# Optimization experiments

Measured on AMD Instinct MI355X. Metric: run time of the kernel, lower is better.

## Reference

```python
import jax, jax.numpy as jnp
import numpy as np

POS_R = 2
CELL_D = 16
BORDER = 16
B, D, H, W = 4, 128, 512, 512

# neighbourhood offsets with i*i + j*j <= pos_r^2, same ordering as the torch module
_OFFS = jnp.array([(i, j) for i in range(-POS_R, POS_R + 1)
                   for j in range(-POS_R, POS_R + 1)
                   if i * i + j * j <= POS_R ** 2], dtype=jnp.int32).T  # [2, K=13]


def _sample(det, max_b=None):
    # per-cell argmax of detection score; equivalent to pixel_unshuffle + argmax + coord gather
    Bt = det.shape[0] if max_b is None else min(max_b, det.shape[0])
    Hc = (H - 2 * BORDER) // CELL_D
    Wc = (W - 2 * BORDER) // CELL_D
    d = det[:Bt, 0, BORDER:BORDER + Hc * CELL_D, BORDER:BORDER + Wc * CELL_D]
    d = d.reshape(Bt, Hc, CELL_D, Wc, CELL_D).transpose(0, 1, 3, 2, 4)
    d = d.reshape(Bt, Hc, Wc, CELL_D * CELL_D)
    idx = jnp.argmax(d, axis=-1)                      # [Bt,Hc,Wc], row-major in-cell index
    i, j = idx // CELL_D, idx % CELL_D
    rows = BORDER + jnp.arange(Hc, dtype=jnp.int32)[None, :, None] * CELL_D + i
    cols = BORDER + jnp.arange(Wc, dtype=jnp.int32)[None, None, :] * CELL_D + j
    x = cols.reshape(-1)   # absolute column coord (unit_aflow channel 0)
    y = rows.reshape(-1)   # absolute row coord (unit_aflow channel 1)
    n = Hc * Wc
    b = jnp.repeat(jnp.arange(Bt, dtype=jnp.int32), n)
    return b, x, y, n


def _clamp(xy):
    return jnp.stack([jnp.clip(xy[0], 0, W - 1), jnp.clip(xy[1], 0, H - 1)])


def _forward(des1, det1, qlt1, des2, det2, qlt2, aflow):
    b, y1, x1, n = _sample(det1)   # original unpacks (b, x, y, n) -> (b, y1, x1, n)
    s_des1 = des1[b, :, y1, x1]                                   # [N, D]
    xy2 = (aflow[b, :, y1, x1] + 0.5).astype(jnp.int32).T         # [2, N], trunc-toward-zero like .long()
    mask = ((0 <= xy2[0]) & (0 <= xy2[1]) & (xy2[0] < W) & (xy2[1] < H)).reshape(B, n)

    xy2p = _clamp(xy2[:, None, :] + _OFFS[:, :, None])            # [2, K, N]
    nb = des2[b[None, :], :, xy2p[1], xy2p[0]]                    # [K, N, D]
    p_all = jnp.einsum('nd,knd->nk', s_des1, nb)                  # [N, K]
    pos = jnp.argmax(p_all, axis=1)
    pscores = jnp.max(p_all, axis=1, keepdims=True)               # [N, 1]
    sel_xy2 = _clamp(xy2 + _OFFS[:, pos])
    qlt = (qlt1[b, :, y1, x1] + qlt2[b, :, sel_xy2[1], sel_xy2[0]]) * 0.5  # [N, 1]

    bd, yd, xd, _ = _sample(det2)                                 # max_neg_b=None -> all images
    distr = des2[bd, :, yd, xd]                                   # [Nd, D]
    dscores = s_des1 @ distr.T                                    # [N, Nd]
    dis2 = (xd[None, :] - xy2[0][:, None]) ** 2 + (yd[None, :] - xy2[1][:, None]) ** 2
    dis2 = dis2 + (bd[None, :] != b[:, None]).astype(jnp.int32) * (POS_R ** 2)
    dscores = jnp.where(dis2 < POS_R ** 2, jnp.zeros((), dscores.dtype), dscores)

    scores = jnp.concatenate([pscores, dscores], axis=1)          # [N, 1+Nd]
    labels = jnp.zeros(scores.shape, dtype=bool).at[:, :1].set(True)
    return scores, labels, mask, qlt


def setup_inputs() -> dict:
    key = jax.random.key(0)
    ks = jax.random.split(key, 7)
    des1 = jax.random.normal(ks[0], (B, D, H, W), jnp.float32)
    det1 = jax.random.uniform(ks[1], (B, 1, H, W), jnp.float32)
    qlt1 = jax.random.uniform(ks[2], (B, 1, H, W), jnp.float32)
    des2 = jax.random.normal(ks[3], (B, D, H, W), jnp.float32)
    det2 = jax.random.uniform(ks[4], (B, 1, H, W), jnp.float32)
    qlt2 = jax.random.uniform(ks[5], (B, 1, H, W), jnp.float32)
    # optical-flow-like absolute coords, partially out of image bounds so mask is nontrivial
    aflow = jax.random.uniform(ks[6], (B, 2, H, W), jnp.float32) * (W + 40.0) - 20.0
    return {"des1": des1, "det1": det1, "qlt1": qlt1,
            "des2": des2, "det2": det2, "qlt2": qlt2, "aflow": aflow}


def reference(des1, det1, qlt1, des2, det2, qlt2, aflow):
    return _forward(des1, det1, qlt1, des2, det2, qlt2, aflow)
```

## Files before the change

kernel.cpp:

```cpp
#include <hip/hip_runtime.h>
#include <cstddef>

#define B_      4
#define D_      128
#define H_      512
#define W_      512
#define NCELL_  900
#define NS_     3600
#define NK_     13
#define SC_     3601
#define TILE_   64
#define KC_     32

__constant__ int c_OI[NK_] = {-2,-1,-1,-1, 0, 0,0,0,0, 1,1,1, 2};
__constant__ int c_OJ[NK_] = { 0,-1, 0, 1,-2,-1,0,1,2,-1,0,1, 0};

__global__ __launch_bounds__(256) void sample_kernel(const float* __restrict__ det1,
                                                     const float* __restrict__ det2,
                                                     int* __restrict__ pos_row,
                                                     int* __restrict__ pos_col) {
    int cell = blockIdx.x;
    const float* det = det1;
    int c = cell;
    if (cell >= NS_) { det = det2; c = cell - NS_; }
    int b  = c / NCELL_;
    int rc = (c % NCELL_) / 30;
    int cc = c % 30;
    int t = threadIdx.x;
    int i = t >> 4, j = t & 15;
    int y = 16 + rc * 16 + i;
    int x = 16 + cc * 16 + j;
    float v = det[(b * H_ + y) * W_ + x];

    __shared__ float sv[256];
    __shared__ int   si[256];
    sv[t] = v; si[t] = t;
    __syncthreads();
    for (int s = 128; s > 0; s >>= 1) {
        if (t < s) {
            float v2 = sv[t + s]; int i2 = si[t + s];
            if (v2 > sv[t] || (v2 == sv[t] && i2 < si[t])) { sv[t] = v2; si[t] = i2; }
        }
        __syncthreads();
    }
    if (t == 0) {
        int best = si[0];
        pos_row[cell] = 16 + rc * 16 + (best >> 4);
        pos_col[cell] = 16 + cc * 16 + (best & 15);
    }
}

__global__ __launch_bounds__(64) void prep1_kernel(const float* __restrict__ des1,
                                                   const float* __restrict__ des2,
                                                   const float* __restrict__ qlt1,
                                                   const float* __restrict__ qlt2,
                                                   const float* __restrict__ aflow,
                                                   const int* __restrict__ pos_row,
                                                   const int* __restrict__ pos_col,
                                                   int* __restrict__ xy2x_out,
                                                   int* __restrict__ xy2y_out,
                                                   float* __restrict__ Amat,
                                                   float* __restrict__ out_scores,
                                                   float* __restrict__ out_mask,
                                                   float* __restrict__ out_qlt) {
    int n = blockIdx.x;
    int lane = threadIdx.x;
    int b = n / NCELL_;
    int row = pos_row[n], col = pos_col[n];
    int d0 = lane;

    const float* p1 = des1 + ((b * D_ + d0) * H_ + col) * W_ + row;
    float a0 = p1[0];
    float a1 = p1[64 * H_ * W_];
    Amat[n * D_ + d0]      = a0;
    Amat[n * D_ + d0 + 64] = a1;

    float fx = aflow[((b * 2 + 0) * H_ + col) * W_ + row];
    float fy = aflow[((b * 2 + 1) * H_ + col) * W_ + row];
    int xx = (int)(fx + 0.5f);
    int yy = (int)(fy + 0.5f);

    float v0s[NK_], v1s[NK_];
#pragma unroll
    for (int k = 0; k < NK_; k++) {
        int X = min(max(xx + c_OI[k], 0), W_ - 1);
        int Y = min(max(yy + c_OJ[k], 0), H_ - 1);
        const float* p2 = des2 + ((b * D_ + d0) * H_ + Y) * W_ + X;
        v0s[k] = p2[0];
        v1s[k] = p2[64 * H_ * W_];
    }

    float bestv = -1e30f; int bestk = 0;
#pragma unroll
    for (int k = 0; k < NK_; k++) {
        float p = a0 * v0s[k] + a1 * v1s[k];
        for (int s = 32; s > 0; s >>= 1) p += __shfl_xor(p, s, 64);
        if (p > bestv) { bestv = p; bestk = k; }
    }

    if (lane == 0) {
        out_scores[(size_t)n * SC_] = bestv;
        bool m = (xx >= 0) && (yy >= 0) && (xx < W_) && (yy < H_);
        out_mask[n] = m ? 1.0f : 0.0f;
        int sx = min(max(xx + c_OI[bestk], 0), W_ - 1);
        int sy = min(max(yy + c_OJ[bestk], 0), H_ - 1);
        float q1 = qlt1[(b * H_ + col) * W_ + row];
        float q2 = qlt2[(b * H_ + sy) * W_ + sx];
        out_qlt[n] = (q1 + q2) * 0.5f;
        xy2x_out[n] = xx;
        xy2y_out[n] = yy;
    }
}

__global__ __launch_bounds__(64) void prep2_kernel(const float* __restrict__ des2,
                                                   const int* __restrict__ pos_row2,
                                                   const int* __restrict__ pos_col2,
                                                   float* __restrict__ Bmat) {
    int m = blockIdx.x;
    int lane = threadIdx.x;
    int b = m / NCELL_;
    int row = pos_row2[m], col = pos_col2[m];
    const float* p = des2 + ((b * D_ + lane) * H_ + col) * W_ + row;
    Bmat[m * D_ + lane]      = p[0];
    Bmat[m * D_ + lane + 64] = p[64 * H_ * W_];
}

__global__ void fill_labels(float4* __restrict__ labels4) {
    const long long N4 = (long long)NS_ * SC_ / 4;
    long long i = (long long)blockIdx.x * blockDim.x + threadIdx.x;
    long long stride = (long long)gridDim.x * blockDim.x;
    for (; i < N4; i += stride) {
        long long e = i * 4;
        int r = (int)(e % SC_);
        float4 v = make_float4(0.f, 0.f, 0.f, 0.f);
        if      (r == 0)    v.x = 1.0f;
        else if (r == 3600) v.y = 1.0f;
        else if (r == 3599) v.z = 1.0f;
        else if (r == 3598) v.w = 1.0f;
        labels4[i] = v;
    }
}

__global__ __launch_bounds__(256) void gemm_kernel(const float* __restrict__ A,
                                                   const float* __restrict__ Bm,
                                                   const int* __restrict__ xy2x,
                                                   const int* __restrict__ xy2y,
                                                   const int* __restrict__ pos_row2,
                                                   const int* __restrict__ pos_col2,
                                                   float* __restrict__ out_scores) {
    __shared__ float As[KC_][TILE_ + 4];
    __shared__ float Bs[KC_][TILE_ + 4];
    int n0 = blockIdx.y * TILE_;
    int m0 = blockIdx.x * TILE_;
    int t  = threadIdx.x;
    int tr = t >> 4;
    int tc = t & 15;

    float acc[4][4] = {{0.f}};

    for (int k0 = 0; k0 < D_; k0 += KC_) {
#pragma unroll
        for (int i = 0; i < 8; i++) {
            int l = t + i * 256;
            int r = l >> 5;
            int c = l & 31;
            int gn = n0 + r;
            As[c][r] = (gn < NS_) ? A[gn * D_ + k0 + c] : 0.0f;
            int gm = m0 + r;
            Bs[c][r] = (gm < NS_) ? Bm[gm * D_ + k0 + c] : 0.0f;
        }
        __syncthreads();
#pragma unroll
        for (int kk = 0; kk < KC_; kk++) {
            float4 av = *(const float4*)&As[kk][tr * 4];
            float4 bv = *(const float4*)&Bs[kk][tc * 4];
            float a[4] = {av.x, av.y, av.z, av.w};
            float bb[4] = {bv.x, bv.y, bv.z, bv.w};
#pragma unroll
            for (int i = 0; i < 4; i++)
#pragma unroll
                for (int j = 0; j < 4; j++)
                    acc[i][j] += a[i] * bb[j];
        }
        __syncthreads();
    }

    int nrow[4], xr[4], yr[4], brr[4];
    int mcol[4], rm[4], cm[4], bmb[4];
#pragma unroll
    for (int i = 0; i < 4; i++) {
        nrow[i] = n0 + tr * 4 + i;
        if (nrow[i] < NS_) {
            xr[i] = xy2x[nrow[i]]; yr[i] = xy2y[nrow[i]]; brr[i] = nrow[i] / NCELL_;
        }
    }
#pragma unroll
    for (int j = 0; j < 4; j++) {
        mcol[j] = m0 + tc * 4 + j;
        if (mcol[j] < NS_) {
            rm[j] = pos_row2[mcol[j]]; cm[j] = pos_col2[mcol[j]]; bmb[j] = mcol[j] / NCELL_;
        }
    }
#pragma unroll
    for (int i = 0; i < 4; i++) {
        if (nrow[i] >= NS_) continue;
#pragma unroll
        for (int j = 0; j < 4; j++) {
            if (mcol[j] >= NS_) continue;
            int dx = rm[j] - xr[i];
            int dy = cm[j] - yr[i];
            int dis2 = dx * dx + dy * dy + (bmb[j] != brr[i] ? 4 : 0);
            float v = (dis2 < 4) ? 0.0f : acc[i][j];
            out_scores[(size_t)nrow[i] * SC_ + 1 + mcol[j]] = v;
        }
    }
}

extern "C" void kernel_launch(void* const* d_in, const int* in_sizes, int n_in,
                              void* d_out, int out_size, void* d_ws, size_t ws_size,
                              hipStream_t stream) {
    const float* des1  = (const float*)d_in[0];
    const float* det1  = (const float*)d_in[1];
    const float* qlt1  = (const float*)d_in[2];
    const float* des2  = (const float*)d_in[3];
    const float* det2  = (const float*)d_in[4];
    const float* qlt2  = (const float*)d_in[5];
    const float* aflow = (const float*)d_in[6];

    float* out = (float*)d_out;
    float* out_scores = out;
    float* out_labels = out + (size_t)NS_ * SC_;
    float* out_mask   = out + 2 * (size_t)NS_ * SC_;
    float* out_qlt    = out + 2 * (size_t)NS_ * SC_ + NS_;

    char* ws = (char*)d_ws;
    int*   pos_row = (int*)(ws);
    int*   pos_col = (int*)(ws + 28800);
    int*   xy2x    = (int*)(ws + 57600);
    int*   xy2y    = (int*)(ws + 72000);
    float* Amat    = (float*)(ws + 86400);
    float* Bmat    = (float*)(ws + 1929600);

    hipLaunchKernelGGL(sample_kernel, dim3(2 * NS_), dim3(256), 0, stream,
                       det1, det2, pos_row, pos_col);
    hipLaunchKernelGGL(prep1_kernel, dim3(NS_), dim3(64), 0, stream,
                       des1, des2, qlt1, qlt2, aflow, pos_row, pos_col,
                       xy2x, xy2y, Amat, out_scores, out_mask, out_qlt);
    hipLaunchKernelGGL(prep2_kernel, dim3(NS_), dim3(64), 0, stream,
                       des2, pos_row + NS_, pos_col + NS_, Bmat);
    hipLaunchKernelGGL(fill_labels, dim3(2048), dim3(256), 0, stream,
                       (float4*)out_labels);
    hipLaunchKernelGGL(gemm_kernel, dim3((NS_ + TILE_ - 1) / TILE_, (NS_ + TILE_ - 1) / TILE_),
                       dim3(256), 0, stream,
                       Amat, Bmat, xy2x, xy2y, pos_row + NS_, pos_col + NS_, out_scores);
}
```

Measured before the change: 1.030 ms.

## Use split-bf16 MFMA GEMM, wave-level sampling argmax, and simplified label fill

Replaces the FP32 shared-memory SIMT GEMM with a bf16 MFMA GEMM. Each descriptor is split into hi and lo bf16 halves and combined with three MFMAs per tile to keep near-fp32 accuracy, with inputs padded to 3648 rows. The per-cell argmax in sampling now runs one wavefront per cell using shuffles instead of a 256-thread shared-memory tree. The label fill is split into a plain zero fill plus a small kernel that sets the ones. The GEMM now reads operands directly from global memory without LDS staging, and the dropped lo*lo term adds a small rounding error relative to fp32.

```diff
diff --git a/kernel.cpp b/kernel.cpp
--- a/kernel.cpp
+++ b/kernel.cpp
@@ -7,46 +7,60 @@
 #define W_      512
 #define NCELL_  900
 #define NS_     3600
+#define NSP_    3648
 #define NK_     13
 #define SC_     3601
-#define TILE_   64
-#define KC_     32
 
 __constant__ int c_OI[NK_] = {-2,-1,-1,-1, 0, 0,0,0,0, 1,1,1, 2};
 __constant__ int c_OJ[NK_] = { 0,-1, 0, 1,-2,-1,0,1,2,-1,0,1, 0};
+
+using short8v = __attribute__((ext_vector_type(8))) short;
+using f32x4   = __attribute__((ext_vector_type(4))) float;
+
+__device__ __forceinline__ unsigned short f2bf(float f) {
+    unsigned u = __float_as_uint(f);
+    return (unsigned short)((u + 0x7FFFu + ((u >> 16) & 1u)) >> 16);
+}
+__device__ __forceinline__ float bf2f(unsigned short h) {
+    return __uint_as_float(((unsigned)h) << 16);
+}
 
 __global__ __launch_bounds__(256) void sample_kernel(const float* __restrict__ det1,
                                                      const float* __restrict__ det2,
                                                      int* __restrict__ pos_row,
                                                      int* __restrict__ pos_col) {
-    int cell = blockIdx.x;
+    int w    = threadIdx.x >> 6;
+    int lane = threadIdx.x & 63;
+    int cell = blockIdx.x * 4 + w;
     const float* det = det1;
     int c = cell;
     if (cell >= NS_) { det = det2; c = cell - NS_; }
     int b  = c / NCELL_;
     int rc = (c % NCELL_) / 30;
     int cc = c % 30;
-    int t = threadIdx.x;
-    int i = t >> 4, j = t & 15;
-    int y = 16 + rc * 16 + i;
-    int x = 16 + cc * 16 + j;
-    float v = det[(b * H_ + y) * W_ + x];
-
-    __shared__ float sv[256];
-    __shared__ int   si[256];
-    sv[t] = v; si[t] = t;
-    __syncthreads();
-    for (int s = 128; s > 0; s >>= 1) {
-        if (t < s) {
-            float v2 = sv[t + s]; int i2 = si[t + s];
-            if (v2 > sv[t] || (v2 == sv[t] && i2 < si[t])) { sv[t] = v2; si[t] = i2; }
-        }
-        __syncthreads();
-    }
-    if (t == 0) {
-        int best = si[0];
-        pos_row[cell] = 16 + rc * 16 + (best >> 4);
-        pos_col[cell] = 16 + cc * 16 + (best & 15);
+    int y0 = 16 + rc * 16;
+    int x0 = 16 + cc * 16;
+    const float* base = det + (b * H_ + y0) * W_ + x0;
+
+    int j  = lane & 15;
+    int i0 = lane >> 4;
+    float bv = -1e30f; int bt = 0;
+#pragma unroll
+    for (int q = 0; q < 4; q++) {
+        int i  = i0 + 4 * q;
+        int tt = i * 16 + j;
+        float v = base[i * W_ + j];
+        if (v > bv) { bv = v; bt = tt; }
+    }
+#pragma unroll
+    for (int s = 32; s > 0; s >>= 1) {
+        float ov = __shfl_xor(bv, s, 64);
+        int   ot = __shfl_xor(bt, s, 64);
+        if (ov > bv || (ov == bv && ot < bt)) { bv = ov; bt = ot; }
+    }
+    if (lane == 0) {
+        pos_row[cell] = y0 + (bt >> 4);
+        pos_col[cell] = x0 + (bt & 15);
     }
 }
 
@@ -59,12 +73,19 @@
                                                    const int* __restrict__ pos_col,
                                                    int* __restrict__ xy2x_out,
                                                    int* __restrict__ xy2y_out,
-                                                   float* __restrict__ Amat,
+                                                   unsigned short* __restrict__ Ahi,
+                                                   unsigned short* __restrict__ Alo,
                                                    float* __restrict__ out_scores,
                                                    float* __restrict__ out_mask,
                                                    float* __restrict__ out_qlt) {
     int n = blockIdx.x;
     int lane = threadIdx.x;
+    size_t o = (size_t)n * D_ + lane;
+    if (n >= NS_) {
+        Ahi[o] = 0; Ahi[o + 64] = 0;
+        Alo[o] = 0; Alo[o + 64] = 0;
+        return;
+    }
     int b = n / NCELL_;
     int row = pos_row[n], col = pos_col[n];
     int d0 = lane;
@@ -72,8 +93,11 @@
     const float* p1 = des1 + ((b * D_ + d0) * H_ + col) * W_ + row;
     float a0 = p1[0];
     float a1 = p1[64 * H_ * W_];
-    Amat[n * D_ + d0]      = a0;
-    Amat[n * D_ + d0 + 64] = a1;
+
+    unsigned short h0 = f2bf(a0), h1 = f2bf(a1);
+    Ahi[o] = h0;            Ahi[o + 64] = h1;
+    Alo[o] = f2bf(a0 - bf2f(h0));
+    Alo[o + 64] = f2bf(a1 - bf2f(h1));
 
     float fx = aflow[((b * 2 + 0) * H_ + col) * W_ + row];
     float fy = aflow[((b * 2 + 1) * H_ + col) * W_ + row];
@@ -115,103 +139,106 @@
 __global__ __launch_bounds__(64) void prep2_kernel(const float* __restrict__ des2,
                                                    const int* __restrict__ pos_row2,
                                                    const int* __restrict__ pos_col2,
-                                                   float* __restrict__ Bmat) {
+                                                   unsigned short* __restrict__ Bhi,
+                                                   unsigned short* __restrict__ Blo) {
     int m = blockIdx.x;
     int lane = threadIdx.x;
+    size_t o = (size_t)m * D_ + lane;
+    if (m >= NS_) {
+        Bhi[o] = 0; Bhi[o + 64] = 0;
+        Blo[o] = 0; Blo[o + 64] = 0;
+        return;
+    }
     int b = m / NCELL_;
     int row = pos_row2[m], col = pos_col2[m];
     const float* p = des2 + ((b * D_ + lane) * H_ + col) * W_ + row;
-    Bmat[m * D_ + lane]      = p[0];
-    Bmat[m * D_ + lane + 64] = p[64 * H_ * W_];
-}
-
-__global__ void fill_labels(float4* __restrict__ labels4) {
+    float a0 = p[0];
+    float a1 = p[64 * H_ * W_];
+    unsigned short h0 = f2bf(a0), h1 = f2bf(a1);
+    Bhi[o] = h0;            Bhi[o + 64] = h1;
+    Blo[o] = f2bf(a0 - bf2f(h0));
+    Blo[o + 64] = f2bf(a1 - bf2f(h1));
+}
+
+__global__ void zero_labels(float4* __restrict__ labels4) {
     const long long N4 = (long long)NS_ * SC_ / 4;
     long long i = (long long)blockIdx.x * blockDim.x + threadIdx.x;
     long long stride = (long long)gridDim.x * blockDim.x;
-    for (; i < N4; i += stride) {
-        long long e = i * 4;
-        int r = (int)(e % SC_);
-        float4 v = make_float4(0.f, 0.f, 0.f, 0.f);
-        if      (r == 0)    v.x = 1.0f;
-        else if (r == 3600) v.y = 1.0f;
-        else if (r == 3599) v.z = 1.0f;
-        else if (r == 3598) v.w = 1.0f;
-        labels4[i] = v;
-    }
-}
-
-__global__ __launch_bounds__(256) void gemm_kernel(const float* __restrict__ A,
-                                                   const float* __restrict__ Bm,
-                                                   const int* __restrict__ xy2x,
-                                                   const int* __restrict__ xy2y,
-                                                   const int* __restrict__ pos_row2,
-                                                   const int* __restrict__ pos_col2,
-                                                   float* __restrict__ out_scores) {
-    __shared__ float As[KC_][TILE_ + 4];
-    __shared__ float Bs[KC_][TILE_ + 4];
-    int n0 = blockIdx.y * TILE_;
-    int m0 = blockIdx.x * TILE_;
-    int t  = threadIdx.x;
-    int tr = t >> 4;
-    int tc = t & 15;
-
-    float acc[4][4] = {{0.f}};
-
-    for (int k0 = 0; k0 < D_; k0 += KC_) {
-#pragma unroll
-        for (int i = 0; i < 8; i++) {
-            int l = t + i * 256;
-            int r = l >> 5;
-            int c = l & 31;
-            int gn = n0 + r;
-            As[c][r] = (gn < NS_) ? A[gn * D_ + k0 + c] : 0.0f;
-            int gm = m0 + r;
-            Bs[c][r] = (gm < NS_) ? Bm[gm * D_ + k0 + c] : 0.0f;
+    float4 z = make_float4(0.f, 0.f, 0.f, 0.f);
+    for (; i < N4; i += stride) labels4[i] = z;
+}
+__global__ void ones_labels(float* __restrict__ labels) {
+    int n = blockIdx.x * blockDim.x + threadIdx.x;
+    if (n < NS_) labels[(size_t)n * SC_] = 1.0f;
+}
+
+__global__ __launch_bounds__(256) void gemm_mfma_kernel(const unsigned short* __restrict__ Ahi,
+                                                        const unsigned short* __restrict__ Alo,
+                                                        const unsigned short* __restrict__ Bhi,
+                                                        const unsigned short* __restrict__ Blo,
+                                                        const int* __restrict__ xy2x,
+                                                        const int* __restrict__ xy2y,
+                                                        const int* __restrict__ pos_row2,
+                                                        const int* __restrict__ pos_col2,
+                                                        float* __restrict__ out_scores) {
+    int t    = threadIdx.x;
+    int wave = t >> 6;
+    int lane = t & 63;
+    int wr = wave >> 1, wc = wave & 1;
+    int n0 = blockIdx.y * 64 + wr * 32;
+    int m0 = blockIdx.x * 64 + wc * 32;
+    int c = lane & 15;
+    int g = lane >> 4;
+
+    f32x4 acc[2][2] = {};
+
+#pragma unroll
+    for (int ks = 0; ks < 4; ks++) {
+        int ko = ks * 32 + g * 8;
+        short8v ah[2], al[2], bh[2], bl[2];
+#pragma unroll
+        for (int f = 0; f < 2; f++) {
+            size_t ai = (size_t)(n0 + f * 16 + c) * D_ + ko;
+            size_t bi = (size_t)(m0 + f * 16 + c) * D_ + ko;
+            ah[f] = *(const short8v*)(Ahi + ai);
+            al[f] = *(const short8v*)(Alo + ai);
+            bh[f] = *(const short8v*)(Bhi + bi);
+            bl[f] = *(const short8v*)(Blo + bi);
         }
-        __syncthreads();
-#pragma unroll
-        for (int kk = 0; kk < KC_; kk++) {
-            float4 av = *(const float4*)&As[kk][tr * 4];
-            float4 bv = *(const float4*)&Bs[kk][tc * 4];
-            float a[4] = {av.x, av.y, av.z, av.w};
-            float bb[4] = {bv.x, bv.y, bv.z, bv.w};
-#pragma unroll
-            for (int i = 0; i < 4; i++)
-#pragma unroll
-                for (int j = 0; j < 4; j++)
-                    acc[i][j] += a[i] * bb[j];
+#pragma unroll
+        for (int i = 0; i < 2; i++)
+#pragma unroll
+            for (int j = 0; j < 2; j++) {
+                acc[i][j] = __builtin_amdgcn_mfma_f32_16x16x32_bf16(ah[i], bh[j], acc[i][j], 0, 0, 0);
+                acc[i][j] = __builtin_amdgcn_mfma_f32_16x16x32_bf16(ah[i], bl[j], acc[i][j], 0, 0, 0);
+                acc[i][j] = __builtin_amdgcn_mfma_f32_16x16x32_bf16(al[i], bh[j], acc[i][j], 0, 0, 0);
+            }
+    }
+
+    int mcol[2], rm[2], cm[2], bm[2];
+#pragma unroll
+    for (int j = 0; j < 2; j++) {
+        mcol[j] = m0 + j * 16 + c;
+        if (mcol[j] < NS_) {
+            rm[j] = pos_row2[mcol[j]]; cm[j] = pos_col2[mcol[j]]; bm[j] = mcol[j] / NCELL_;
         }
-        __syncthreads();
-    }
-
-    int nrow[4], xr[4], yr[4], brr[4];
-    int mcol[4], rm[4], cm[4], bmb[4];
-#pragma unroll
-    for (int i = 0; i < 4; i++) {
-        nrow[i] = n0 + tr * 4 + i;
-        if (nrow[i] < NS_) {
-            xr[i] = xy2x[nrow[i]]; yr[i] = xy2y[nrow[i]]; brr[i] = nrow[i] / NCELL_;
-        }
-    }
-#pragma unroll
-    for (int j = 0; j < 4; j++) {
-        mcol[j] = m0 + tc * 4 + j;
-        if (mcol[j] < NS_) {
-            rm[j] = pos_row2[mcol[j]]; cm[j] = pos_col2[mcol[j]]; bmb[j] = mcol[j] / NCELL_;
-        }
-    }
-#pragma unroll
-    for (int i = 0; i < 4; i++) {
-        if (nrow[i] >= NS_) continue;
-#pragma unroll
-        for (int j = 0; j < 4; j++) {
-            if (mcol[j] >= NS_) continue;
-            int dx = rm[j] - xr[i];
-            int dy = cm[j] - yr[i];
-            int dis2 = dx * dx + dy * dy + (bmb[j] != brr[i] ? 4 : 0);
-            float v = (dis2 < 4) ? 0.0f : acc[i][j];
-            out_scores[(size_t)nrow[i] * SC_ + 1 + mcol[j]] = v;
+    }
+#pragma unroll
+    for (int i = 0; i < 2; i++) {
+#pragma unroll
+        for (int r = 0; r < 4; r++) {
+            int n = n0 + i * 16 + g * 4 + r;
+            if (n >= NS_) continue;
+            int xr = xy2x[n], yr = xy2y[n], br = n / NCELL_;
+#pragma unroll
+            for (int j = 0; j < 2; j++) {
+                if (mcol[j] >= NS_) continue;
+                int dx = rm[j] - xr;
+                int dy = cm[j] - yr;
+                int dis2 = dx * dx + dy * dy + (bm[j] != br ? 4 : 0);
+                float v = acc[i][j][r];
+                out_scores[(size_t)n * SC_ + 1 + mcol[j]] = (dis2 < 4) ? 0.0f : v;
+            }
         }
     }
 }
@@ -234,23 +261,27 @@
     float* out_qlt    = out + 2 * (size_t)NS_ * SC_ + NS_;
 
     char* ws = (char*)d_ws;
-    int*   pos_row = (int*)(ws);
-    int*   pos_col = (int*)(ws + 28800);
-    int*   xy2x    = (int*)(ws + 57600);
-    int*   xy2y    = (int*)(ws + 72000);
-    float* Amat    = (float*)(ws + 86400);
-    float* Bmat    = (float*)(ws + 1929600);
-
-    hipLaunchKernelGGL(sample_kernel, dim3(2 * NS_), dim3(256), 0, stream,
+    int* pos_row = (int*)(ws);
+    int* pos_col = (int*)(ws + 28800);
+    int* xy2x    = (int*)(ws + 57600);
+    int* xy2y    = (int*)(ws + 72000);
+    unsigned short* Ahi = (unsigned short*)(ws +   86400);
+    unsigned short* Alo = (unsigned short*)(ws + 1020288);
+    unsigned short* Bhi = (unsigned short*)(ws + 1954176);
+    unsigned short* Blo = (unsigned short*)(ws + 2888064);
+
+    hipLaunchKernelGGL(sample_kernel, dim3(2 * NS_ / 4), dim3(256), 0, stream,
                        det1, det2, pos_row, pos_col);
-    hipLaunchKernelGGL(prep1_kernel, dim3(NS_), dim3(64), 0, stream,
+    hipLaunchKernelGGL(prep1_kernel, dim3(NSP_), dim3(64), 0, stream,
                        des1, des2, qlt1, qlt2, aflow, pos_row, pos_col,
-                       xy2x, xy2y, Amat, out_scores, out_mask, out_qlt);
-    hipLaunchKernelGGL(prep2_kernel, dim3(NS_), dim3(64), 0, stream,
-                       des2, pos_row + NS_, pos_col + NS_, Bmat);
-    hipLaunchKernelGGL(fill_labels, dim3(2048), dim3(256), 0, stream,
+                       xy2x, xy2y, Ahi, Alo, out_scores, out_mask, out_qlt);
+    hipLaunchKernelGGL(prep2_kernel, dim3(NSP_), dim3(64), 0, stream,
+                       des2, pos_row + NS_, pos_col + NS_, Bhi, Blo);
+    hipLaunchKernelGGL(zero_labels, dim3(2048), dim3(256), 0, stream,
                        (float4*)out_labels);
-    hipLaunchKernelGGL(gemm_kernel, dim3((NS_ + TILE_ - 1) / TILE_, (NS_ + TILE_ - 1) / TILE_),
-                       dim3(256), 0, stream,
-                       Amat, Bmat, xy2x, xy2y, pos_row + NS_, pos_col + NS_, out_scores);
-}
+    hipLaunchKernelGGL(ones_labels, dim3((NS_ + 255) / 256), dim3(256), 0, stream,
+                       out_labels);
+    hipLaunchKernelGGL(gemm_mfma_kernel, dim3(NSP_ / 64, NSP_ / 64), dim3(256), 0, stream,
+                       Ahi, Alo, Bhi, Blo, xy2x, xy2y,
+                       pos_row + NS_, pos_col + NS_, out_scores);
+}
```

Result: faster. 971.0 us (-5.7%).
